# Kernel tuning notes

Hardware: AMD Instinct MI355X
Metric: run time of the kernel (lower is better)

The kernel has to match this reference:

```python
import jax, jax.numpy as jnp
import numpy as np

D_MODEL = 256; D_STATE = 32; D_INNER = 512; DT_RANK = 16
BATCH = 8; SEQ = 512
EPS = 1e-5

def _silu(x):
    return x * jax.nn.sigmoid(x)

def _mamba(x, Win, convw, convb, Wx, Wdt, dtb, Alog, Dp, Wout):
    # x: [B, L, d_model]
    Bsz, L, _ = x.shape
    d_inner, N = Alog.shape
    K = convw.shape[1]
    xz = x @ Win.T                              # [B, L, 2*d_inner]
    xi, z = jnp.split(xz, 2, axis=-1)
    # causal depthwise conv1d (left pad K-1)
    xc = jax.lax.conv_general_dilated(
        xi.transpose(0, 2, 1), convw[:, None, :], (1,), [(K - 1, 0)],
        feature_group_count=d_inner, dimension_numbers=('NCH', 'OIH', 'NCH'))
    xi = _silu(xc.transpose(0, 2, 1) + convb)   # [B, L, d_inner]
    x_dbl = xi @ Wx.T                           # [B, L, dt_rank + 2N]
    dt, Bm, Cm = jnp.split(x_dbl, [DT_RANK, DT_RANK + N], axis=-1)
    dt = jax.nn.softplus(dt @ Wdt.T + dtb)      # [B, L, d_inner]
    A = -jnp.exp(Alog)                          # [d_inner, N]

    def step(h, inp):
        dt_t, B_t, C_t, x_t = inp               # [B,d], [B,N], [B,N], [B,d]
        dA = jnp.exp(dt_t[..., None] * A)       # [B, d_inner, N]
        h = dA * h + (dt_t * x_t)[..., None] * B_t[:, None, :]
        y = jnp.einsum('bdn,bn->bd', h, C_t)
        return h, y

    h0 = jnp.zeros((Bsz, d_inner, N), x.dtype)
    xs = (dt.transpose(1, 0, 2), Bm.transpose(1, 0, 2),
          Cm.transpose(1, 0, 2), xi.transpose(1, 0, 2))
    _, ys = jax.lax.scan(step, h0, xs)
    y = ys.transpose(1, 0, 2) + xi * Dp
    return (y * _silu(z)) @ Wout.T

def _forward(x, ln_g, ln_b, ml, mg, gate_W, gate_b, op_W, op_b):
    mu = x.mean(-1, keepdims=True)
    var = ((x - mu) ** 2).mean(-1, keepdims=True)
    xn = (x - mu) / jnp.sqrt(var + EPS) * ln_g + ln_b
    xr = jnp.flip(xn, axis=1)
    f_fwd = _mamba(xn, *ml) + _mamba(xn, *mg)
    f_rev = jnp.flip(_mamba(xr, *ml) + _mamba(xr, *mg), axis=1)
    gate = jax.nn.sigmoid(jnp.concatenate([f_fwd, f_rev], -1) @ gate_W.T + gate_b)
    fused = gate * f_fwd + (1 - gate) * f_rev
    return fused @ op_W.T + op_b  # dropout: identity in eval

def setup_inputs():
    key = jax.random.key(0)
    ks = iter(jax.random.split(key, 48))
    def w(shape, s=0.02):
        return jax.random.normal(next(ks), shape, jnp.float32) * s
    def mamba_params(dconv):
        return {
            'Win': w((2 * D_INNER, D_MODEL)),
            'convw': w((D_INNER, dconv), 0.2),
            'convb': w((D_INNER,), 0.01),
            'Wx': w((DT_RANK + 2 * D_STATE, D_INNER)),
            'Wdt': w((D_INNER, DT_RANK), 0.1),
            'dtb': w((D_INNER,), 0.5),
            'Alog': jnp.log(jnp.broadcast_to(
                jnp.arange(1, D_STATE + 1, dtype=jnp.float32), (D_INNER, D_STATE))),
            'Dp': jnp.ones((D_INNER,), jnp.float32),
            'Wout': w((D_MODEL, D_INNER)),
        }
    inp = {'x': jax.random.normal(next(ks), (BATCH, SEQ, D_MODEL), jnp.float32),
           'ln_g': jnp.ones((D_MODEL,), jnp.float32),
           'ln_b': jnp.zeros((D_MODEL,), jnp.float32)}
    for pre, dconv in (('ml_', 4), ('mg_', 8)):
        for k, v in mamba_params(dconv).items():
            inp[pre + k] = v
    inp['gate_W'] = w((D_MODEL, 2 * D_MODEL))
    inp['gate_b'] = jnp.zeros((D_MODEL,), jnp.float32)
    inp['op_W'] = w((D_MODEL, D_MODEL))
    inp['op_b'] = jnp.zeros((D_MODEL,), jnp.float32)
    return inp

def reference(x, ln_g, ln_b,
              ml_Win, ml_convw, ml_convb, ml_Wx, ml_Wdt, ml_dtb, ml_Alog, ml_Dp, ml_Wout,
              mg_Win, mg_convw, mg_convb, mg_Wx, mg_Wdt, mg_dtb, mg_Alog, mg_Dp, mg_Wout,
              gate_W, gate_b, op_W, op_b):
    ml = (ml_Win, ml_convw, ml_convb, ml_Wx, ml_Wdt, ml_dtb, ml_Alog, ml_Dp, ml_Wout)
    mg = (mg_Win, mg_convw, mg_convb, mg_Wx, mg_Wdt, mg_dtb, mg_Alog, mg_Dp, mg_Wout)
    return _forward(x, ln_g, ln_b, ml, mg, gate_W, gate_b, op_W, op_b)
```

## Files before the change

### kernel.cpp

```cpp
#include <hip/hip_runtime.h>
#include <math.h>

#define L_SEQ 512
#define NB 8
#define DM 256
#define DI 512
#define NSTATE 32
#define DTR 16
#define R_ROWS 4096

typedef unsigned short ushort_t;
typedef __bf16 bf16t;
typedef bf16t bf16x8 __attribute__((ext_vector_type(8)));
typedef float f32x4 __attribute__((ext_vector_type(4)));

static __device__ __forceinline__ float siluf(float x){
  return x / (1.f + __expf(-x));
}
static __device__ __forceinline__ ushort_t f2bf(float f){
  unsigned u = __float_as_uint(f);
  u += 0x7fff + ((u>>16)&1);
  return (ushort_t)(u>>16);
}
static __device__ __forceinline__ float bf2f(ushort_t h){
  return __uint_as_float(((unsigned)h)<<16);
}

__global__ __launch_bounds__(256) void prep_weights(
  const float* __restrict__ Wi0, const float* __restrict__ Wi1,
  const float* __restrict__ Wx0, const float* __restrict__ Wx1,
  const float* __restrict__ Wo0, const float* __restrict__ Wo1,
  const float* __restrict__ gW,  const float* __restrict__ oW,
  ushort_t* WiH0, ushort_t* WiL0, ushort_t* WiH1, ushort_t* WiL1,
  ushort_t* WxH0, ushort_t* WxL0, ushort_t* WxH1, ushort_t* WxL1,
  ushort_t* WoH,  ushort_t* WoL,  ushort_t* gH, ushort_t* gL,
  ushort_t* oH, ushort_t* oL)
{
  int i = blockIdx.x*256 + threadIdx.x;
  float v; ushort_t *ph, *pl; int oi;
  if (i < 262144){ v = Wi0[i]; ph=WiH0; pl=WiL0; oi=i; }
  else if (i < 524288){ oi=i-262144; v = Wi1[oi]; ph=WiH1; pl=WiL1; }
  else if (i < 565248){ oi=i-524288; v = Wx0[oi]; ph=WxH0; pl=WxL0; }
  else if (i < 606208){ oi=i-565248; v = Wx1[oi]; ph=WxH1; pl=WxL1; }
  else if (i < 868352){ oi=i-606208; int n=oi>>10, k=oi&1023;
                        v = (k<512)? Wo0[n*512+k] : Wo1[n*512+k-512];
                        ph=WoH; pl=WoL; }
  else if (i < 999424){ oi=i-868352; v = gW[oi]; ph=gH; pl=gL; }
  else { oi=i-999424; v = oW[oi]; ph=oH; pl=oL; }
  ushort_t h = f2bf(v);
  ph[oi] = h;
  pl[oi] = f2bf(v - bf2f(h));
}

__global__ __launch_bounds__(256) void ln_kernel(const float* __restrict__ x,
    const float* __restrict__ g, const float* __restrict__ b,
    ushort_t* __restrict__ xnh, ushort_t* __restrict__ xnl)
{
  int row = blockIdx.x*4 + (threadIdx.x>>6);
  int lane = threadIdx.x & 63;
  const float* xr = x + (size_t)row*DM;
  float v0 = xr[lane], v1 = xr[lane+64], v2 = xr[lane+128], v3 = xr[lane+192];
  float s = v0+v1+v2+v3;
  #pragma unroll
  for (int m=1;m<64;m<<=1) s += __shfl_xor(s, m);
  float mu = s*(1.f/DM);
  float d0=v0-mu,d1=v1-mu,d2=v2-mu,d3=v3-mu;
  float vs = d0*d0+d1*d1+d2*d2+d3*d3;
  #pragma unroll
  for (int m=1;m<64;m<<=1) vs += __shfl_xor(vs, m);
  float rstd = rsqrtf(vs*(1.f/DM)+1e-5f);
  size_t ro = (size_t)row*DM;
  #pragma unroll
  for (int j=0;j<4;j++){
    int c = lane + j*64;
    float val = (j==0?d0:j==1?d1:j==2?d2:d3)*rstd*g[c] + b[c];
    ushort_t h = f2bf(val);
    xnh[ro+c] = h;
    xnl[ro+c] = f2bf(val - bf2f(h));
  }
}

template<int BM, int EPI>
__global__ __launch_bounds__(256) void gemm_mfma(
    const ushort_t* __restrict__ Ahi, const ushort_t* __restrict__ Alo, long Az,
    const ushort_t* __restrict__ Bhi, const ushort_t* __restrict__ Blo,
    int K, int N,
    float* __restrict__ C, int ldc, int Czoff,
    ushort_t* __restrict__ Phi, ushort_t* __restrict__ Plo, int ldp,
    const float* __restrict__ bias)
{
  constexpr int MT = (BM==128)?4:2;
  __shared__ ushort_t Al[BM][64];
  __shared__ ushort_t Bl[128][64];
  int tid = threadIdx.x;
  int z = blockIdx.z;
  const ushort_t* Ah = Ahi + (long)z*Az;
  const ushort_t* Alw = Alo + (long)z*Az;
  float* Cz = C + (long)z*Czoff;
  int bm0 = blockIdx.y*BM, bn0 = blockIdx.x*128;

  int w = tid>>6, l = tid&63;
  int wm = w>>1, wn = w&1;
  int lr = l&15, q = l>>4;

  f32x4 acc[MT][4];
  #pragma unroll
  for (int i=0;i<MT;i++)
    #pragma unroll
    for (int j=0;j<4;j++) acc[i][j] = (f32x4){0.f,0.f,0.f,0.f};

  for (int k0=0; k0<K; k0+=32){
    #pragma unroll
    for (int p=0; p<BM/32; ++p){
      int idx = p*256 + tid;
      int row = idx>>3, c8 = idx&7;
      int kq = c8>>1, pl = c8&1;
      const ushort_t* src = (pl? Alw : Ah) + (long)(bm0+row)*K + k0 + kq*8;
      uint4 v = *(const uint4*)src;
      *(uint4*)&Al[row][(c8 ^ (row&7))<<3] = v;
    }
    #pragma unroll
    for (int p=0; p<4; ++p){
      int idx = p*256 + tid;
      int row = idx>>3, c8 = idx&7;
      int kq = c8>>1, pl = c8&1;
      int rn = bn0+row; if (rn > N-1) rn = N-1;
      const ushort_t* src = (pl? Blo : Bhi) + (long)rn*K + k0 + kq*8;
      uint4 v = *(const uint4*)src;
      *(uint4*)&Bl[row][(c8 ^ (row&7))<<3] = v;
    }
    __syncthreads();
    bf16x8 bh[4], bl[4];
    #pragma unroll
    for (int nt=0; nt<4; ++nt){
      int r = wn*64 + nt*16 + lr;
      bh[nt] = *(const bf16x8*)&Bl[r][((2*q)   ^ (r&7))<<3];
      bl[nt] = *(const bf16x8*)&Bl[r][((2*q+1) ^ (r&7))<<3];
    }
    #pragma unroll
    for (int mt=0; mt<MT; ++mt){
      int r = wm*(BM/2) + mt*16 + lr;
      bf16x8 ah = *(const bf16x8*)&Al[r][((2*q)   ^ (r&7))<<3];
      bf16x8 al = *(const bf16x8*)&Al[r][((2*q+1) ^ (r&7))<<3];
      #pragma unroll
      for (int nt=0; nt<4; ++nt){
        acc[mt][nt] = __builtin_amdgcn_mfma_f32_16x16x32_bf16(al, bh[nt], acc[mt][nt], 0,0,0);
        acc[mt][nt] = __builtin_amdgcn_mfma_f32_16x16x32_bf16(ah, bl[nt], acc[mt][nt], 0,0,0);
        acc[mt][nt] = __builtin_amdgcn_mfma_f32_16x16x32_bf16(ah, bh[nt], acc[mt][nt], 0,0,0);
      }
    }
    __syncthreads();
  }
  #pragma unroll
  for (int mt=0; mt<MT; ++mt){
    #pragma unroll
    for (int nt=0; nt<4; ++nt){
      #pragma unroll
      for (int r=0; r<4; ++r){
        int row = bm0 + wm*(BM/2) + mt*16 + q*4 + r;
        int col = bn0 + wn*64 + nt*16 + lr;
        if (col < N){
          float v = acc[mt][nt][r];
          if (EPI==1) v += bias[col];
          Cz[(long)row*ldc + col] = v;
          if (EPI==2){
            ushort_t h = f2bf(v);
            (Phi + (long)z*Czoff)[(long)row*ldp + col] = h;
            (Plo + (long)z*Czoff)[(long)row*ldp + col] = f2bf(v - bf2f(h));
          }
        }
      }
    }
  }
}

template<int KC>
__global__ __launch_bounds__(256) void conv_kernel(
  const float* __restrict__ xz, const float* __restrict__ w, const float* __restrict__ cb,
  float* __restrict__ xi, ushort_t* __restrict__ xih, ushort_t* __restrict__ xil)
{
  int idx = blockIdx.x*256 + threadIdx.x;
  int c = idx & (DI-1);
  int t = (idx >> 9) & (L_SEQ-1);
  int bb = idx >> 18;
  const float* base = xz + ((size_t)bb*L_SEQ)*1024 + c;
  float wr[KC];
  #pragma unroll
  for (int j=0;j<KC;j++) wr[j] = w[c*KC+j];
  float bias = cb[c];
  float accF = bias, accR = bias;
  #pragma unroll
  for (int j=0;j<KC;j++){
    int tf = t - (KC-1) + j;
    if (tf >= 0)     accF += wr[j]*base[(size_t)tf*1024];
    int tr = t + (KC-1) - j;
    if (tr < L_SEQ)  accR += wr[j]*base[(size_t)tr*1024];
  }
  const size_t RD = (size_t)R_ROWS*DI;
  float sF = siluf(accF), sR = siluf(accR);
  xi[idx] = sF; xi[RD+idx] = sR;
  ushort_t hF = f2bf(sF), hR = f2bf(sR);
  xih[idx] = hF;      xil[idx] = f2bf(sF - bf2f(hF));
  xih[RD+idx] = hR;   xil[RD+idx] = f2bf(sR - bf2f(hR));
}

__global__ __launch_bounds__(256) void scan_kernel(
  const float* __restrict__ xd,
  const float* __restrict__ xi,
  const float* __restrict__ xz,
  const float* __restrict__ WdtW,
  const float* __restrict__ dtb,
  const float* __restrict__ Alog,
  const float* __restrict__ Dp,
  ushort_t* __restrict__ yh, ushort_t* __restrict__ yl, int col0)
{
  int bi = blockIdx.x;
  int dir = bi >> 9, b = (bi >> 6) & 7, d0 = (bi & 63) * 8;
  const float* xdp = xd + (size_t)dir*R_ROWS*80;
  const float* xip = xi + (size_t)dir*R_ROWS*DI;
  ushort_t* yoh = yh + (size_t)dir*R_ROWS*1024 + col0;
  ushort_t* yol = yl + (size_t)dir*R_ROWS*1024 + col0;
  size_t bL = (size_t)b*L_SEQ;

  __shared__ float  XD[32][84];
  __shared__ float  HC[8][16][36];
  __shared__ float2 DTs[32][8];
  __shared__ float2 XZs[32][8];
  __shared__ float  YO[32][8];
  __shared__ float  WT[16][8];
  __shared__ float  DTB[8], DPS[8];

  int tid = threadIdx.x;
  if (tid < 128){ int k = tid>>3, cc = tid&7; WT[k][cc] = WdtW[(d0+cc)*DTR + k]; }
  else if (tid < 136) DTB[tid-128] = dtb[d0 + tid-128];
  else if (tid < 144) DPS[tid-136] = Dp[d0 + tid-136];

  int wv = tid>>6, l64 = tid&63;
  int ch = wv*2 + (l64>>5);
  int n  = l64 & 31;
  float Al = -__expf(Alog[(d0+ch)*NSTATE + n]) * 1.44269504089f;
  float h = 0.f;

  int li8 = tid>>3, c8 = tid&7;
  int chD = tid>>5, t2 = tid&31;

  for (int chunk=0; chunk<16; ++chunk){
    int s0 = chunk*32;
    if (chunk){
      int st = s0 - 32 + li8;
      int t = dir ? (L_SEQ-1-st) : st;
      float v = YO[li8][c8];
      ushort_t hh = f2bf(v);
      yoh[(bL + t)*1024 + d0 + c8] = hh;
      yol[(bL + t)*1024 + d0 + c8] = f2bf(v - bf2f(hh));
    }
    {
      int rr = tid>>3, ee = tid&7;
      int st = s0 + rr; int t = dir ? (L_SEQ-1-st) : st;
      const float* src = xdp + (bL + t)*80;
      #pragma unroll
      for (int j=0;j<10;j++) XD[rr][ee + j*8] = src[ee + j*8];
      XZs[li8][c8] = make_float2(xip[(bL + t)*DI + d0 + c8],
                                 xz[(bL + t)*1024 + DI + d0 + c8]);
    }
    __syncthreads();
    {
      float s = DTB[c8];
      #pragma unroll
      for (int k=0;k<DTR;k++) s = fmaf(XD[li8][k], WT[k][c8], s);
      float dtv = fmaxf(s,0.f) + log1pf(__expf(-fabsf(s)));
      DTs[li8][c8] = make_float2(dtv, dtv * XZs[li8][c8].x);
    }
    __syncthreads();
    #pragma unroll
    for (int half=0; half<2; ++half){
      #pragma unroll
      for (int li=0; li<16; ++li){
        int li2 = half*16 + li;
        float2 dd = DTs[li2][ch];
        float Bv = XD[li2][DTR + n];
        float Cv = XD[li2][DTR + NSTATE + n];
        float dA = __builtin_amdgcn_exp2f(dd.x * Al);
        h = fmaf(dA, h, dd.y * Bv);
        HC[ch][li][n] = h * Cv;
      }
      __syncthreads();
      {
        int t = t2 >> 1, nh = t2 & 1;
        const float* hp = &HC[chD][t][nh*16];
        float4 s1 = *(const float4*)&hp[0];
        float4 s2 = *(const float4*)&hp[4];
        float4 s3 = *(const float4*)&hp[8];
        float4 s4 = *(const float4*)&hp[12];
        float ssum = ((s1.x+s1.y)+(s1.z+s1.w)) + ((s2.x+s2.y)+(s2.z+s2.w))
                   + ((s3.x+s3.y)+(s3.z+s3.w)) + ((s4.x+s4.y)+(s4.z+s4.w));
        ssum += __shfl_xor(ssum, 1);
        if (!nh){
          int li2 = half*16 + t;
          float2 xzv = XZs[li2][chD];
          YO[li2][chD] = (ssum + xzv.x * DPS[chD]) * siluf(xzv.y);
        }
      }
      __syncthreads();
    }
  }
  {
    int st = 480 + li8;
    int t = dir ? (L_SEQ-1-st) : st;
    float v = YO[li8][c8];
    ushort_t hh = f2bf(v);
    yoh[(bL + t)*1024 + d0 + c8] = hh;
    yol[(bL + t)*1024 + d0 + c8] = f2bf(v - bf2f(hh));
  }
}

__global__ __launch_bounds__(256) void fuse_kernel(const float* __restrict__ gpre,
   const float* __restrict__ gb, const float* __restrict__ ffr,
   ushort_t* __restrict__ fush, ushort_t* __restrict__ fusl)
{
  int idx = blockIdx.x*256 + threadIdx.x;
  int r = idx >> 8, c = idx & (DM-1);
  size_t ro = (size_t)r*2*DM;
  float ffv = ffr[ro + c];
  float frv = ffr[ro + DM + c];
  float g = 1.f/(1.f+__expf(-(gpre[idx] + gb[c])));
  float v = g*ffv + (1.f-g)*frv;
  ushort_t h = f2bf(v);
  fush[idx] = h;
  fusl[idx] = f2bf(v - bf2f(h));
}

extern "C" void kernel_launch(void* const* d_in, const int* in_sizes, int n_in,
                              void* d_out, int out_size, void* d_ws, size_t ws_size,
                              hipStream_t stream)
{
  (void)in_sizes; (void)n_in; (void)out_size; (void)ws_size;
  const float* x    = (const float*)d_in[0];
  const float* ln_g = (const float*)d_in[1];
  const float* ln_b = (const float*)d_in[2];
  const float* Win[2]  = {(const float*)d_in[3],  (const float*)d_in[12]};
  const float* convw[2]= {(const float*)d_in[4],  (const float*)d_in[13]};
  const float* convb[2]= {(const float*)d_in[5],  (const float*)d_in[14]};
  const float* Wx[2]   = {(const float*)d_in[6],  (const float*)d_in[15]};
  const float* Wdt[2]  = {(const float*)d_in[7],  (const float*)d_in[16]};
  const float* dtb[2]  = {(const float*)d_in[8],  (const float*)d_in[17]};
  const float* Alog[2] = {(const float*)d_in[9],  (const float*)d_in[18]};
  const float* Dpp[2]  = {(const float*)d_in[10], (const float*)d_in[19]};
  const float* Wout[2] = {(const float*)d_in[11], (const float*)d_in[20]};
  const float* gate_W = (const float*)d_in[21];
  const float* gate_b = (const float*)d_in[22];
  const float* op_W   = (const float*)d_in[23];
  const float* op_b   = (const float*)d_in[24];
  float* out = (float*)d_out;

  char* wsb = (char*)d_ws;
  size_t off = 0;
  auto allocB = [&](size_t bytes)->char*{
    char* p = wsb + off; off += (bytes + 15) & ~size_t(15); return p; };
  const size_t R = R_ROWS;

  float* xzb  = (float*)allocB(R*1024*4);
  float* xi   = (float*)allocB(2*R*DI*4);
  float* xdd  = (float*)allocB(2*R*80*4);
  float* ffr  = (float*)allocB(R*2*DM*4);
  float* gpre = (float*)allocB(R*DM*4);
  ushort_t* xnh = (ushort_t*)allocB(R*DM*2);
  ushort_t* xnl = (ushort_t*)allocB(R*DM*2);
  ushort_t* xih = (ushort_t*)allocB(2*R*DI*2);
  ushort_t* xil = (ushort_t*)allocB(2*R*DI*2);
  ushort_t* yhp = (ushort_t*)allocB(2*R*1024*2);
  ushort_t* ylp = (ushort_t*)allocB(2*R*1024*2);
  ushort_t* ffh = (ushort_t*)allocB(R*2*DM*2);
  ushort_t* ffl = (ushort_t*)allocB(R*2*DM*2);
  ushort_t* fsh = (ushort_t*)allocB(R*DM*2);
  ushort_t* fsl = (ushort_t*)allocB(R*DM*2);
  ushort_t* WiH[2] = {(ushort_t*)allocB(262144*2), (ushort_t*)allocB(262144*2)};
  ushort_t* WiL[2] = {(ushort_t*)allocB(262144*2), (ushort_t*)allocB(262144*2)};
  ushort_t* WxH[2] = {(ushort_t*)allocB(40960*2),  (ushort_t*)allocB(40960*2)};
  ushort_t* WxL[2] = {(ushort_t*)allocB(40960*2),  (ushort_t*)allocB(40960*2)};
  ushort_t* WoH = (ushort_t*)allocB(262144*2);
  ushort_t* WoL = (ushort_t*)allocB(262144*2);
  ushort_t* gH  = (ushort_t*)allocB(131072*2);
  ushort_t* gL  = (ushort_t*)allocB(131072*2);
  ushort_t* oH  = (ushort_t*)allocB(65536*2);
  ushort_t* oL  = (ushort_t*)allocB(65536*2);

  prep_weights<<<4160, 256, 0, stream>>>(Win[0], Win[1], Wx[0], Wx[1],
      Wout[0], Wout[1], gate_W, op_W,
      WiH[0], WiL[0], WiH[1], WiL[1], WxH[0], WxL[0], WxH[1], WxL[1],
      WoH, WoL, gH, gL, oH, oL);

  ln_kernel<<<R/4, 256, 0, stream>>>(x, ln_g, ln_b, xnh, xnl);

  for (int m=0; m<2; ++m){
    gemm_mfma<128,0><<<dim3(8, 32, 1), 256, 0, stream>>>(
        xnh, xnl, 0, WiH[m], WiL[m], DM, 1024, xzb, 1024, 0,
        nullptr, nullptr, 0, nullptr);
    if (m==0) conv_kernel<4><<<8192,256,0,stream>>>(xzb, convw[m], convb[m], xi, xih, xil);
    else      conv_kernel<8><<<8192,256,0,stream>>>(xzb, convw[m], convb[m], xi, xih, xil);
    gemm_mfma<64,0><<<dim3(1, 128, 1), 256, 0, stream>>>(
        xih, xil, 0, WxH[m], WxL[m], DI, 80, xdd, 80, 0,
        nullptr, nullptr, 0, nullptr);
    scan_kernel<<<1024, 256, 0, stream>>>(xdd, xi, xzb, Wdt[m], dtb[m], Alog[m], Dpp[m],
                                          yhp, ylp, m*512);
  }
  gemm_mfma<128,2><<<dim3(2, 32, 2), 256, 0, stream>>>(
      yhp, ylp, (long)R*1024, WoH, WoL, 1024, 256, ffr, 2*DM, DM,
      ffh, ffl, 2*DM, nullptr);
  gemm_mfma<64,0><<<dim3(2, 64, 1), 256, 0, stream>>>(
      ffh, ffl, 0, gH, gL, 2*DM, DM, gpre, DM, 0,
      nullptr, nullptr, 0, nullptr);
  fuse_kernel<<<R*DM/256, 256, 0, stream>>>(gpre, gate_b, ffr, fsh, fsl);
  gemm_mfma<64,1><<<dim3(2, 64, 1), 256, 0, stream>>>(
      fsh, fsl, 0, oH, oL, DM, DM, out, DM, 0,
      nullptr, nullptr, 0, op_b);
}
```

Measured before the change: 465.9 us.

## Restructure scan to reduce via DPP, split dt/BC outputs, vectorize conv

The scan kernel now reduces h*C across the 32 state lanes with DPP row operations instead of staging partial products in shared memory and syncing twice per half-chunk. B and C are read straight from global memory, interleaved by a new GEMM epilogue that writes dt and B/C into separate buffers. The dt projection moves into registers with float4 loads. The conv kernel handles four channels per thread with float4 loads and stores. This cuts barriers and shared-memory traffic, at the cost of per-step global loads of B/C inside the serial recurrence.

After: 620.1 us. +33.1%, slower.

```diff
diff --git a/kernel.cpp b/kernel.cpp
--- a/kernel.cpp
+++ b/kernel.cpp
@@ -24,6 +24,11 @@
 }
 static __device__ __forceinline__ float bf2f(ushort_t h){
   return __uint_as_float(((unsigned)h)<<16);
+}
+template<int CTRL>
+static __device__ __forceinline__ float dpp_add(float v){
+  int t = __builtin_amdgcn_update_dpp(0, __float_as_int(v), CTRL, 0xF, 0xF, true);
+  return v + __int_as_float(t);
 }
 
 __global__ __launch_bounds__(256) void prep_weights(
@@ -87,7 +92,7 @@
     int K, int N,
     float* __restrict__ C, int ldc, int Czoff,
     ushort_t* __restrict__ Phi, ushort_t* __restrict__ Plo, int ldp,
-    const float* __restrict__ bias)
+    const float* __restrict__ bias, float* __restrict__ C2)
 {
   constexpr int MT = (BM==128)?4:2;
   __shared__ ushort_t Al[BM][64];
@@ -161,12 +166,18 @@
         int col = bn0 + wn*64 + nt*16 + lr;
         if (col < N){
           float v = acc[mt][nt][r];
-          if (EPI==1) v += bias[col];
-          Cz[(long)row*ldc + col] = v;
-          if (EPI==2){
-            ushort_t h = f2bf(v);
-            (Phi + (long)z*Czoff)[(long)row*ldp + col] = h;
-            (Plo + (long)z*Czoff)[(long)row*ldp + col] = f2bf(v - bf2f(h));
+          if (EPI==4){
+            if (col < DTR)      C [(long)row*16 + col] = v;
+            else if (col < 48)  C2[(long)row*64 + 2*(col-DTR)] = v;
+            else                C2[(long)row*64 + 2*(col-48) + 1] = v;
+          } else {
+            if (EPI==1) v += bias[col];
+            Cz[(long)row*ldc + col] = v;
+            if (EPI==2){
+              ushort_t h = f2bf(v);
+              (Phi + (long)z*Czoff)[(long)row*ldp + col] = h;
+              (Plo + (long)z*Czoff)[(long)row*ldp + col] = f2bf(v - bf2f(h));
+            }
           }
         }
       }
@@ -180,32 +191,55 @@
   float* __restrict__ xi, ushort_t* __restrict__ xih, ushort_t* __restrict__ xil)
 {
   int idx = blockIdx.x*256 + threadIdx.x;
-  int c = idx & (DI-1);
-  int t = (idx >> 9) & (L_SEQ-1);
-  int bb = idx >> 18;
-  const float* base = xz + ((size_t)bb*L_SEQ)*1024 + c;
-  float wr[KC];
-  #pragma unroll
-  for (int j=0;j<KC;j++) wr[j] = w[c*KC+j];
-  float bias = cb[c];
-  float accF = bias, accR = bias;
+  int c4 = (idx & 127) * 4;
+  int t  = (idx >> 7) & (L_SEQ-1);
+  int bb = idx >> 16;
+  const float* base = xz + ((size_t)bb*L_SEQ)*1024 + c4;
+  float4 wr[KC];
+  #pragma unroll
+  for (int j=0;j<KC;j++)
+    wr[j] = make_float4(w[(c4+0)*KC+j], w[(c4+1)*KC+j],
+                        w[(c4+2)*KC+j], w[(c4+3)*KC+j]);
+  float4 bias = *(const float4*)&cb[c4];
+  float4 aF = bias, aR = bias;
   #pragma unroll
   for (int j=0;j<KC;j++){
     int tf = t - (KC-1) + j;
-    if (tf >= 0)     accF += wr[j]*base[(size_t)tf*1024];
+    if (tf >= 0){
+      float4 v = *(const float4*)&base[(size_t)tf*1024];
+      aF.x = fmaf(wr[j].x, v.x, aF.x); aF.y = fmaf(wr[j].y, v.y, aF.y);
+      aF.z = fmaf(wr[j].z, v.z, aF.z); aF.w = fmaf(wr[j].w, v.w, aF.w);
+    }
     int tr = t + (KC-1) - j;
-    if (tr < L_SEQ)  accR += wr[j]*base[(size_t)tr*1024];
-  }
+    if (tr < L_SEQ){
+      float4 v = *(const float4*)&base[(size_t)tr*1024];
+      aR.x = fmaf(wr[j].x, v.x, aR.x); aR.y = fmaf(wr[j].y, v.y, aR.y);
+      aR.z = fmaf(wr[j].z, v.z, aR.z); aR.w = fmaf(wr[j].w, v.w, aR.w);
+    }
+  }
+  float4 sF = make_float4(siluf(aF.x), siluf(aF.y), siluf(aF.z), siluf(aF.w));
+  float4 sR = make_float4(siluf(aR.x), siluf(aR.y), siluf(aR.z), siluf(aR.w));
   const size_t RD = (size_t)R_ROWS*DI;
-  float sF = siluf(accF), sR = siluf(accR);
-  xi[idx] = sF; xi[RD+idx] = sR;
-  ushort_t hF = f2bf(sF), hR = f2bf(sR);
-  xih[idx] = hF;      xil[idx] = f2bf(sF - bf2f(hF));
-  xih[RD+idx] = hR;   xil[RD+idx] = f2bf(sR - bf2f(hR));
+  size_t o = ((size_t)bb*L_SEQ + t)*DI + c4;
+  *(float4*)&xi[o]    = sF;
+  *(float4*)&xi[RD+o] = sR;
+  ushort_t fh0=f2bf(sF.x), fh1=f2bf(sF.y), fh2=f2bf(sF.z), fh3=f2bf(sF.w);
+  ushort_t rh0=f2bf(sR.x), rh1=f2bf(sR.y), rh2=f2bf(sR.z), rh3=f2bf(sR.w);
+  uint2 pF = make_uint2((unsigned)fh0 | ((unsigned)fh1<<16), (unsigned)fh2 | ((unsigned)fh3<<16));
+  uint2 pR = make_uint2((unsigned)rh0 | ((unsigned)rh1<<16), (unsigned)rh2 | ((unsigned)rh3<<16));
+  *(uint2*)&xih[o]    = pF;
+  *(uint2*)&xih[RD+o] = pR;
+  uint2 lF = make_uint2((unsigned)f2bf(sF.x-bf2f(fh0)) | ((unsigned)f2bf(sF.y-bf2f(fh1))<<16),
+                        (unsigned)f2bf(sF.z-bf2f(fh2)) | ((unsigned)f2bf(sF.w-bf2f(fh3))<<16));
+  uint2 lR = make_uint2((unsigned)f2bf(sR.x-bf2f(rh0)) | ((unsigned)f2bf(sR.y-bf2f(rh1))<<16),
+                        (unsigned)f2bf(sR.z-bf2f(rh2)) | ((unsigned)f2bf(sR.w-bf2f(rh3))<<16));
+  *(uint2*)&xil[o]    = lF;
+  *(uint2*)&xil[RD+o] = lR;
 }
 
 __global__ __launch_bounds__(256) void scan_kernel(
-  const float* __restrict__ xd,
+  const float* __restrict__ dtIn,
+  const float* __restrict__ bcI,
   const float* __restrict__ xi,
   const float* __restrict__ xz,
   const float* __restrict__ WdtW,
@@ -216,98 +250,101 @@
 {
   int bi = blockIdx.x;
   int dir = bi >> 9, b = (bi >> 6) & 7, d0 = (bi & 63) * 8;
-  const float* xdp = xd + (size_t)dir*R_ROWS*80;
-  const float* xip = xi + (size_t)dir*R_ROWS*DI;
+  const float* dtp = dtIn + (size_t)dir*R_ROWS*16;
+  const float* bcp = bcI  + (size_t)dir*R_ROWS*64;
+  const float* xip = xi   + (size_t)dir*R_ROWS*DI;
   ushort_t* yoh = yh + (size_t)dir*R_ROWS*1024 + col0;
   ushort_t* yol = yl + (size_t)dir*R_ROWS*1024 + col0;
   size_t bL = (size_t)b*L_SEQ;
 
-  __shared__ float  XD[32][84];
-  __shared__ float  HC[8][16][36];
-  __shared__ float2 DTs[32][8];
-  __shared__ float2 XZs[32][8];
-  __shared__ float  YO[32][8];
-  __shared__ float  WT[16][8];
-  __shared__ float  DTB[8], DPS[8];
+  __shared__ float  dtA[8][36];
+  __shared__ float  dxA[8][36];
+  __shared__ float2 XZt[8][36];
+  __shared__ float  YOT[8][36];
 
   int tid = threadIdx.x;
-  if (tid < 128){ int k = tid>>3, cc = tid&7; WT[k][cc] = WdtW[(d0+cc)*DTR + k]; }
-  else if (tid < 136) DTB[tid-128] = dtb[d0 + tid-128];
-  else if (tid < 144) DPS[tid-136] = Dp[d0 + tid-136];
-
   int wv = tid>>6, l64 = tid&63;
   int ch = wv*2 + (l64>>5);
   int n  = l64 & 31;
-  float Al = -__expf(Alog[(d0+ch)*NSTATE + n]) * 1.44269504089f;
+  int li8 = tid>>3, c8 = tid&7;
+
+  float Al  = -__expf(Alog[(d0+ch)*NSTATE + n]) * 1.44269504089f;
+  float Dpv = Dp[d0+ch];
+  const float4* wp = (const float4*)&WdtW[(d0+c8)*DTR];
+  float4 w0 = wp[0], w1 = wp[1], w2 = wp[2], w3 = wp[3];
+  float dtbv = dtb[d0+c8];
+  bool writer = (l64==16) || (l64==48);
   float h = 0.f;
-
-  int li8 = tid>>3, c8 = tid&7;
-  int chD = tid>>5, t2 = tid&31;
 
   for (int chunk=0; chunk<16; ++chunk){
     int s0 = chunk*32;
     if (chunk){
       int st = s0 - 32 + li8;
       int t = dir ? (L_SEQ-1-st) : st;
-      float v = YO[li8][c8];
+      float v = YOT[c8][li8];
       ushort_t hh = f2bf(v);
       yoh[(bL + t)*1024 + d0 + c8] = hh;
       yol[(bL + t)*1024 + d0 + c8] = f2bf(v - bf2f(hh));
     }
     {
-      int rr = tid>>3, ee = tid&7;
-      int st = s0 + rr; int t = dir ? (L_SEQ-1-st) : st;
-      const float* src = xdp + (bL + t)*80;
+      int st = s0 + li8;
+      int t = dir ? (L_SEQ-1-st) : st;
+      size_t row = bL + t;
+      const float4* dp = (const float4*)&dtp[row*16];
+      float4 a0 = dp[0], a1 = dp[1], a2 = dp[2], a3 = dp[3];
+      float s = dtbv;
+      s = fmaf(a0.x,w0.x, fmaf(a0.y,w0.y, fmaf(a0.z,w0.z, fmaf(a0.w,w0.w, s))));
+      s = fmaf(a1.x,w1.x, fmaf(a1.y,w1.y, fmaf(a1.z,w1.z, fmaf(a1.w,w1.w, s))));
+      s = fmaf(a2.x,w2.x, fmaf(a2.y,w2.y, fmaf(a2.z,w2.z, fmaf(a2.w,w2.w, s))));
+      s = fmaf(a3.x,w3.x, fmaf(a3.y,w3.y, fmaf(a3.z,w3.z, fmaf(a3.w,w3.w, s))));
+      float dtv = fmaxf(s,0.f) + log1pf(__expf(-fabsf(s)));
+      float xiv = xip[row*DI + d0 + c8];
+      float zv  = xz[row*1024 + DI + d0 + c8];
+      dtA[c8][li8] = dtv;
+      dxA[c8][li8] = dtv * xiv;
+      XZt[c8][li8] = make_float2(xiv, zv);
+    }
+    __syncthreads();
+    #pragma unroll
+    for (int g=0; g<8; ++g){
+      int t4 = g*4;
+      float4 dt4 = *(const float4*)&dtA[ch][t4];
+      float4 dx4 = *(const float4*)&dxA[ch][t4];
+      float ys0, ys1, ys2, ys3;
       #pragma unroll
-      for (int j=0;j<10;j++) XD[rr][ee + j*8] = src[ee + j*8];
-      XZs[li8][c8] = make_float2(xip[(bL + t)*DI + d0 + c8],
-                                 xz[(bL + t)*1024 + DI + d0 + c8]);
+      for (int s=0; s<4; ++s){
+        int st = s0 + t4 + s;
+        int t = dir ? (L_SEQ-1-st) : st;
+        float2 bc = *(const float2*)&bcp[(bL + t)*64 + 2*n];
+        float dtv = (s==0)?dt4.x:(s==1)?dt4.y:(s==2)?dt4.z:dt4.w;
+        float dxv = (s==0)?dx4.x:(s==1)?dx4.y:(s==2)?dx4.z:dx4.w;
+        float dA = __builtin_amdgcn_exp2f(dtv * Al);
+        h = fmaf(dA, h, dxv * bc.x);
+        float yp = h * bc.y;
+        yp = dpp_add<0xB1>(yp);
+        yp = dpp_add<0x4E>(yp);
+        yp = dpp_add<0x141>(yp);
+        yp = dpp_add<0x140>(yp);
+        yp = dpp_add<0x142>(yp);
+        if (s==0) ys0=yp; else if (s==1) ys1=yp; else if (s==2) ys2=yp; else ys3=yp;
+      }
+      if (writer){
+        float4 p0 = *(const float4*)&XZt[ch][t4];
+        float4 p1 = *(const float4*)&XZt[ch][t4+2];
+        float4 yo;
+        yo.x = (ys0 + p0.x*Dpv) * siluf(p0.y);
+        yo.y = (ys1 + p0.z*Dpv) * siluf(p0.w);
+        yo.z = (ys2 + p1.x*Dpv) * siluf(p1.y);
+        yo.w = (ys3 + p1.z*Dpv) * siluf(p1.w);
+        *(float4*)&YOT[ch][t4] = yo;
+      }
     }
     __syncthreads();
-    {
-      float s = DTB[c8];
-      #pragma unroll
-      for (int k=0;k<DTR;k++) s = fmaf(XD[li8][k], WT[k][c8], s);
-      float dtv = fmaxf(s,0.f) + log1pf(__expf(-fabsf(s)));
-      DTs[li8][c8] = make_float2(dtv, dtv * XZs[li8][c8].x);
-    }
-    __syncthreads();
-    #pragma unroll
-    for (int half=0; half<2; ++half){
-      #pragma unroll
-      for (int li=0; li<16; ++li){
-        int li2 = half*16 + li;
-        float2 dd = DTs[li2][ch];
-        float Bv = XD[li2][DTR + n];
-        float Cv = XD[li2][DTR + NSTATE + n];
-        float dA = __builtin_amdgcn_exp2f(dd.x * Al);
-        h = fmaf(dA, h, dd.y * Bv);
-        HC[ch][li][n] = h * Cv;
-      }
-      __syncthreads();
-      {
-        int t = t2 >> 1, nh = t2 & 1;
-        const float* hp = &HC[chD][t][nh*16];
-        float4 s1 = *(const float4*)&hp[0];
-        float4 s2 = *(const float4*)&hp[4];
-        float4 s3 = *(const float4*)&hp[8];
-        float4 s4 = *(const float4*)&hp[12];
-        float ssum = ((s1.x+s1.y)+(s1.z+s1.w)) + ((s2.x+s2.y)+(s2.z+s2.w))
-                   + ((s3.x+s3.y)+(s3.z+s3.w)) + ((s4.x+s4.y)+(s4.z+s4.w));
-        ssum += __shfl_xor(ssum, 1);
-        if (!nh){
-          int li2 = half*16 + t;
-          float2 xzv = XZs[li2][chD];
-          YO[li2][chD] = (ssum + xzv.x * DPS[chD]) * siluf(xzv.y);
-        }
-      }
-      __syncthreads();
-    }
   }
   {
     int st = 480 + li8;
     int t = dir ? (L_SEQ-1-st) : st;
-    float v = YO[li8][c8];
+    float v = YOT[c8][li8];
     ushort_t hh = f2bf(v);
     yoh[(bL + t)*1024 + d0 + c8] = hh;
     yol[(bL + t)*1024 + d0 + c8] = f2bf(v - bf2f(hh));
@@ -361,7 +398,8 @@
 
   float* xzb  = (float*)allocB(R*1024*4);
   float* xi   = (float*)allocB(2*R*DI*4);
-  float* xdd  = (float*)allocB(2*R*80*4);
+  float* dtIn = (float*)allocB(2*R*16*4);
+  float* bcI  = (float*)allocB(2*R*64*4);
   float* ffr  = (float*)allocB(R*2*DM*4);
   float* gpre = (float*)allocB(R*DM*4);
   ushort_t* xnh = (ushort_t*)allocB(R*DM*2);
@@ -395,23 +433,23 @@
   for (int m=0; m<2; ++m){
     gemm_mfma<128,0><<<dim3(8, 32, 1), 256, 0, stream>>>(
         xnh, xnl, 0, WiH[m], WiL[m], DM, 1024, xzb, 1024, 0,
-        nullptr, nullptr, 0, nullptr);
-    if (m==0) conv_kernel<4><<<8192,256,0,stream>>>(xzb, convw[m], convb[m], xi, xih, xil);
-    else      conv_kernel<8><<<8192,256,0,stream>>>(xzb, convw[m], convb[m], xi, xih, xil);
-    gemm_mfma<64,0><<<dim3(1, 128, 1), 256, 0, stream>>>(
-        xih, xil, 0, WxH[m], WxL[m], DI, 80, xdd, 80, 0,
-        nullptr, nullptr, 0, nullptr);
-    scan_kernel<<<1024, 256, 0, stream>>>(xdd, xi, xzb, Wdt[m], dtb[m], Alog[m], Dpp[m],
+        nullptr, nullptr, 0, nullptr, nullptr);
+    if (m==0) conv_kernel<4><<<2048,256,0,stream>>>(xzb, convw[m], convb[m], xi, xih, xil);
+    else      conv_kernel<8><<<2048,256,0,stream>>>(xzb, convw[m], convb[m], xi, xih, xil);
+    gemm_mfma<64,4><<<dim3(1, 128, 1), 256, 0, stream>>>(
+        xih, xil, 0, WxH[m], WxL[m], DI, 80, dtIn, 16, 0,
+        nullptr, nullptr, 0, nullptr, bcI);
+    scan_kernel<<<1024, 256, 0, stream>>>(dtIn, bcI, xi, xzb, Wdt[m], dtb[m], Alog[m], Dpp[m],
                                           yhp, ylp, m*512);
   }
   gemm_mfma<128,2><<<dim3(2, 32, 2), 256, 0, stream>>>(
       yhp, ylp, (long)R*1024, WoH, WoL, 1024, 256, ffr, 2*DM, DM,
-      ffh, ffl, 2*DM, nullptr);
+      ffh, ffl, 2*DM, nullptr, nullptr);
   gemm_mfma<64,0><<<dim3(2, 64, 1), 256, 0, stream>>>(
       ffh, ffl, 0, gH, gL, 2*DM, DM, gpre, DM, 0,
-      nullptr, nullptr, 0, nullptr);
+      nullptr, nullptr, 0, nullptr, nullptr);
   fuse_kernel<<<R*DM/256, 256, 0, stream>>>(gpre, gate_b, ffr, fsh, fsl);
   gemm_mfma<64,1><<<dim3(2, 64, 1), 256, 0, stream>>>(
       fsh, fsl, 0, oH, oL, DM, DM, out, DM, 0,
-      nullptr, nullptr, 0, op_b);
-}
+      nullptr, nullptr, 0, op_b, nullptr);
+}
```
